# Performance work log

Measured on AMD Instinct MI355X. Metric: run time of the kernel, lower is better.

The kernel has to match this reference:

```python
import jax, jax.numpy as jnp
import numpy as np

# FPN level layout for a 1024x1024 input image
LEVEL_HW = [(128, 128), (64, 64), (32, 32), (16, 16), (8, 8)]
STRIDES = [8, 16, 32, 64, 128]
IMG = 1024.0
NUM_CLASSES = 80
SCORE_THRESH = 0.2
NMS_THRESH = 0.6
TOPK = 1000
DETS = 100
BATCH = 8
TOTAL = sum(h * w for h, w in LEVEL_HW)  # 21824


def _make_anchors():
    rows = []
    for (h, w), s in zip(LEVEL_HW, STRIDES):
        xs = (np.arange(w, dtype=np.float32) + 0.5) * s
        ys = (np.arange(h, dtype=np.float32) + 0.5) * s
        xx, yy = np.meshgrid(xs, ys, indexing='ij')  # x-major, matches transpose(2,3) flatten
        pts = np.stack([xx.ravel(), yy.ravel(), xx.ravel(), yy.ravel()], axis=1)
        rows.append(pts)
    return np.concatenate(rows, axis=0).astype(np.float32)


def setup_inputs() -> dict:
    key = jax.random.key(0)
    k1, k2, k3 = jax.random.split(key, 3)
    cls_logits = jax.random.normal(k1, (BATCH, TOTAL, NUM_CLASSES), dtype=jnp.float32)
    bbox_regression = jax.random.uniform(k2, (BATCH, TOTAL, 4), dtype=jnp.float32) * 64.0
    bbox_ctrness = jax.random.normal(k3, (BATCH, TOTAL, 1), dtype=jnp.float32)
    anchors = jnp.asarray(_make_anchors())
    return {"cls_logits": cls_logits, "bbox_regression": bbox_regression,
            "bbox_ctrness": bbox_ctrness, "anchors": anchors}


def _iou_matrix(b):
    # b: [N,4] -> [N,N] pairwise IoU
    area = jnp.clip(b[:, 2] - b[:, 0], 0) * jnp.clip(b[:, 3] - b[:, 1], 0)
    lt = jnp.maximum(b[:, None, :2], b[None, :, :2])
    rb = jnp.minimum(b[:, None, 2:], b[None, :, 2:])
    wh = jnp.clip(rb - lt, 0)
    inter = wh[..., 0] * wh[..., 1]
    union = area[:, None] + area[None, :] - inter
    return inter / jnp.maximum(union, 1e-9)


def _postprocess_one(logits, reg, ctr, anchors):
    boxes_l, scores_l, labels_l = [], [], []
    off = 0
    for (h, w) in LEVEL_HW:
        n = h * w
        lg = logits[off:off + n]          # [n, C]
        rg = reg[off:off + n]             # [n, 4]
        ct = ctr[off:off + n, 0]          # [n]
        an = anchors[off:off + n]         # [n, 4]
        vals = lg.max(axis=-1)
        cls = jnp.argmax(lg, axis=-1)
        sc = jnp.sqrt(jax.nn.sigmoid(vals) * jax.nn.sigmoid(ct))
        # masked threshold + top-k  ==  filter-then-topk of the original
        masked = jnp.where(sc > SCORE_THRESH, sc, -1.0)
        k = min(TOPK, n)
        tv, ti = jax.lax.top_k(masked, k)
        a = an[ti]
        r = rg[ti]
        cx = (a[:, 0] + a[:, 2]) * 0.5
        cy = (a[:, 1] + a[:, 3]) * 0.5
        bx = jnp.stack([cx - r[:, 0], cy - r[:, 1], cx + r[:, 2], cy + r[:, 3]], axis=-1)
        bx = jnp.clip(bx, 0.0, IMG)       # clip_boxes_to_image
        boxes_l.append(bx)
        scores_l.append(tv)
        labels_l.append(cls[ti])
        off += n
    boxes = jnp.concatenate(boxes_l, axis=0)    # [N,4], N=3320
    scores = jnp.concatenate(scores_l, axis=0)  # [N]
    labels = jnp.concatenate(labels_l, axis=0)  # [N]
    N = boxes.shape[0]
    valid = scores > SCORE_THRESH
    order = jnp.argsort(-scores)
    boxes = boxes[order]
    scores = scores[order]
    labels = labels[order]
    valid = valid[order]
    # batched_nms: offset boxes per class so cross-class IoU is 0
    boff = boxes + (labels.astype(boxes.dtype) * (IMG + 1.0))[:, None]
    iou = _iou_matrix(boff)
    idx = jnp.arange(N)
    def body(i, active):
        sup = (iou[i] > NMS_THRESH) & (idx > i) & active[i]
        return active & ~sup
    active = jax.lax.fori_loop(0, N, body, valid)
    fsc = jnp.where(active, scores, -jnp.inf)
    tv, ti = jax.lax.top_k(fsc, DETS)
    m = tv > SCORE_THRESH
    out_boxes = jnp.where(m[:, None], boxes[ti], 0.0)
    out_scores = jnp.where(m, tv, 0.0)
    out_labels = jnp.where(m, labels[ti], -1)
    return out_boxes, out_scores, out_labels


def reference(cls_logits, bbox_regression, bbox_ctrness, anchors):
    fn = lambda l, r, c: _postprocess_one(l, r, c, anchors)
    boxes, scores, labels = jax.vmap(fn)(cls_logits, bbox_regression, bbox_ctrness)
    return boxes, scores, labels
```

## Files before the change

kernel.cpp:

```cpp
#include <hip/hip_runtime.h>
#include <stdint.h>

typedef unsigned long long u64;
typedef unsigned int u32;

#define BATCH   8
#define TOTAL   21824
#define NCLS    80
#define NDET    100
#define IMGSZ   1024.0f
#define STHR    0.2f
#define NMST    0.6f
#define NBUCK   2048
#define BMAX    2015
#define KGLOB   1000
#define NLOC    22

__device__ __forceinline__ float sigm(float x) { return 1.0f / (1.0f + expf(-x)); }

__device__ __forceinline__ u32 mapKm(float s) {
    u32 u = __float_as_uint(s);
    u32 m = u ^ ((u & 0x80000000u) ? 0xFFFFFFFFu : 0x80000000u);
    return ~m;
}
__device__ __forceinline__ u64 makeKey(float s, u32 idx) {
    return (((u64)mapKm(s)) << 32) | (u64)idx;
}

__device__ __forceinline__ int bucketOfV(float s) {
    int b = (int)(__fmul_rn(__fsub_rn(1.0f, s), 2520.0f));
    return b > BMAX ? BMAX : b;
}

__device__ __forceinline__ bool suppress(float4 a, float4 c) {
    float aa = __fmul_rn(fmaxf(__fsub_rn(a.z, a.x), 0.f), fmaxf(__fsub_rn(a.w, a.y), 0.f));
    float ac = __fmul_rn(fmaxf(__fsub_rn(c.z, c.x), 0.f), fmaxf(__fsub_rn(c.w, c.y), 0.f));
    float ltx = fmaxf(a.x, c.x), lty = fmaxf(a.y, c.y);
    float rbx = fminf(a.z, c.z), rby = fminf(a.w, c.w);
    float iw = fmaxf(__fsub_rn(rbx, ltx), 0.f), ih = fmaxf(__fsub_rn(rby, lty), 0.f);
    float inter = __fmul_rn(iw, ih);
    float uni = __fsub_rn(__fadd_rn(aa, ac), inter);
    float iou = __fdiv_rn(inter, fmaxf(uni, 1e-9f));
    return iou > NMST;
}

__global__ __launch_bounds__(256) void zero_hist(u32* __restrict__ g) {
    ((uint4*)g)[blockIdx.x * 256 + threadIdx.x] = make_uint4(0u, 0u, 0u, 0u);
}

__global__ __launch_bounds__(256) void score_kernel(
        const float* __restrict__ logits, const float* __restrict__ ctr,
        float* __restrict__ mscore, int* __restrict__ mlabel,
        u32* __restrict__ ghist) {
    const int b = blockIdx.y;
    const int tid = threadIdx.x;
    const int wave = tid >> 6, lane = tid & 63;
    const int g = lane >> 2, j = lane & 3;
    const int rowBase = blockIdx.x * 256 + wave * 64;
#pragma unroll
    for (int t = 0; t < 4; t++) {
        int r = rowBase + 16 * t + g;
        bool valid = r < TOTAL;
        float best = -1e30f; int bi = 0;
        if (valid) {
            const float* rowp = logits + ((size_t)b * TOTAL + r) * NCLS + j * 4;
#pragma unroll
            for (int u = 0; u < 5; u++) {
                float4 v = *(const float4*)(rowp + u * 16);
                int c0 = u * 16 + j * 4;
                if (v.x > best) { best = v.x; bi = c0; }
                if (v.y > best) { best = v.y; bi = c0 + 1; }
                if (v.z > best) { best = v.z; bi = c0 + 2; }
                if (v.w > best) { best = v.w; bi = c0 + 3; }
            }
        }
#pragma unroll
        for (int off = 1; off <= 2; off <<= 1) {
            float ob = __shfl_xor(best, off);
            int obi = __shfl_xor(bi, off);
            if (ob > best || (ob == best && obi < bi)) { best = ob; bi = obi; }
        }
        if (valid && j == 0) {
            float c = ctr[(size_t)b * TOTAL + r];
            float sc = sqrtf(sigm(best) * sigm(c));
            bool pass = sc > STHR;
            mscore[(size_t)b * TOTAL + r] = pass ? sc : -1.0f;
            mlabel[(size_t)b * TOTAL + r] = bi;
            if (pass) atomicAdd(&ghist[(size_t)b * NBUCK + bucketOfV(sc)], 1u);
        }
    }
}

__global__ __launch_bounds__(1024) void nms_kernel(
        const float* __restrict__ mscore, const int* __restrict__ mlabel,
        const float* __restrict__ anchors, const float* __restrict__ reg,
        const u32* __restrict__ ghist, float* __restrict__ out) {
    __shared__ u32 cur[NBUCK];
    __shared__ u64 skey[2048];
    __shared__ u32 waveSum[16], waveOff[16];
    __shared__ u32 sh_B, sh_m;
    __shared__ int s_count;
    __shared__ int accI[NDET];
    __shared__ float4 accB[NDET];
    __shared__ float4 accR[NDET];
    __shared__ int wIdx[64];
    __shared__ float4 wb[64], wraw[64];
    __shared__ u64 wsup[64];
    __shared__ u32 s_rej32[2];

    const int b = blockIdx.x, tid = threadIdx.x;
    const int wave = tid >> 6, lane = tid & 63;
    const float* ms = mscore + (size_t)b * TOTAL;

    uint2 hv = ((const uint2*)(ghist + (size_t)b * NBUCK))[tid];

    float sv[NLOC];
#pragma unroll
    for (int k = 0; k < NLOC; k++) {
        int i = tid + (k << 10);
        sv[k] = (i < TOTAL) ? ms[i] : -1.0f;
    }

    u32 h0 = hv.x, h1 = hv.y;
    u32 s = h0 + h1;
    u32 incl = s;
    for (int o = 1; o < 64; o <<= 1) {
        u32 t2 = (u32)__shfl_up((int)incl, o);
        if (lane >= o) incl += t2;
    }
    if (lane == 63) waveSum[wave] = incl;
    __syncthreads();
    if (tid == 0) {
        u32 acc = 0;
#pragma unroll
        for (int w = 0; w < 16; w++) { waveOff[w] = acc; acc += waveSum[w]; }
        sh_m = acc;
        sh_B = (u32)BMAX;
        s_count = 0;
    }
    __syncthreads();
    const u32 E = waveOff[wave] + incl - s;
    if (E < KGLOB && KGLOB <= E + h0)            { sh_B = (u32)(2 * tid);     sh_m = E + h0; }
    else if (E + h0 < KGLOB && KGLOB <= E + h0 + h1) { sh_B = (u32)(2 * tid + 1); sh_m = E + h0 + h1; }
    cur[2 * tid] = E;
    cur[2 * tid + 1] = E + h0;
    __syncthreads();
    const int Bstar = (int)sh_B;

#pragma unroll
    for (int k = 0; k < NLOC; k++) {
        float s0 = sv[k];
        if (s0 > STHR) {
            int bk = bucketOfV(s0);
            if (bk <= Bstar) {
                int pos = (int)atomicAdd(&cur[bk], 1u);
                if (pos < 2048) skey[pos] = makeKey(s0, (u32)(tid + (k << 10)));
            }
        }
    }
    __syncthreads();

#pragma unroll
    for (int q = 0; q < 2; q++) {
        int bk = 2 * tid + q;
        u32 cnt = q ? h1 : h0;
        if (bk <= Bstar && cnt > 1) {
            int lo = (int)(q ? (E + h0) : E);
            int hi = lo + (int)cnt; if (hi > 2048) hi = 2048;
            for (int i2 = lo + 1; i2 < hi; i2++) {
                u64 key = skey[i2];
                int j2 = i2 - 1;
                while (j2 >= lo && skey[j2] > key) { skey[j2 + 1] = skey[j2]; j2--; }
                skey[j2 + 1] = key;
            }
        }
    }
    __syncthreads();
    int m = (int)sh_m; if (m > 2048) m = 2048;

    int count = 0, Ew = 0;
    while (true) {
        int take = m - Ew; if (take > 64) take = 64;
        if (take <= 0) break;

        if (tid < take) {
            int idx = (int)(skey[Ew + tid] & 0xFFFFFFFFu);
            float4 a = ((const float4*)anchors)[idx];
            float4 r = ((const float4*)reg)[(size_t)b * TOTAL + idx];
            float cx = (a.x + a.z) * 0.5f;
            float cy = (a.y + a.w) * 0.5f;
            float x1 = fminf(fmaxf(cx - r.x, 0.0f), IMGSZ);
            float y1 = fminf(fmaxf(cy - r.y, 0.0f), IMGSZ);
            float x2 = fminf(fmaxf(cx + r.z, 0.0f), IMGSZ);
            float y2 = fminf(fmaxf(cy + r.w, 0.0f), IMGSZ);
            float4 raw = make_float4(x1, y1, x2, y2);
            float off = (float)mlabel[(size_t)b * TOTAL + idx] * (IMGSZ + 1.0f);
            float4 ob = make_float4(__fadd_rn(x1, off), __fadd_rn(y1, off),
                                    __fadd_rn(x2, off), __fadd_rn(y2, off));
            wraw[tid] = raw; wb[tid] = ob; wIdx[tid] = idx;
        }
        if (tid < 2) s_rej32[tid] = 0;
        __syncthreads();

        {
            bool rej = false;
            if (lane < take) {
                for (int s2 = wave; s2 < count; s2 += 16) {
                    if (suppress(accB[s2], wb[lane])) { rej = true; break; }
                }
            }
            u64 mask = __ballot(rej);
            if (lane == 0 && mask) {
                u32 lo = (u32)mask, hi = (u32)(mask >> 32);
                if (lo) atomicOr(&s_rej32[0], lo);
                if (hi) atomicOr(&s_rej32[1], hi);
            }
        }
        for (int rr = wave; rr < take; rr += 16) {
            bool sp = false;
            if (lane < take && lane > rr) sp = suppress(wb[rr], wb[lane]);
            u64 mask = __ballot(sp);
            if (lane == 0) wsup[rr] = mask;
        }
        __syncthreads();

        if (wave == 0) {
            u64 supr = (lane < take) ? wsup[lane] : 0;
            u64 rejM = (u64)s_rej32[0] | ((u64)s_rej32[1] << 32);
            u64 aliveM = ((take >= 64) ? ~0ull : ((1ull << take) - 1ull)) & ~rejM;
            u64 accM = 0;
            for (int rr = 0; rr < take; rr++) {
                if ((aliveM >> rr) & 1) {
                    accM |= 1ull << rr;
                    u64 sr = __shfl(supr, rr);
                    aliveM &= ~sr;
                }
            }
            int na = __popcll(accM);
            int space = NDET - count;
            int takeA = na < space ? na : space;
            if (lane < take && ((accM >> lane) & 1)) {
                int pos = __popcll(accM & ((1ull << lane) - 1ull));
                if (pos < takeA) {
                    accI[count + pos] = wIdx[lane];
                    accB[count + pos] = wb[lane];
                    accR[count + pos] = wraw[lane];
                }
            }
            if (lane == 0) s_count = count + takeA;
        }
        __syncthreads();
        count = s_count;
        Ew += take;
        if (count >= NDET) break;
    }
    __syncthreads();

    for (int s2 = tid; s2 < NDET; s2 += 1024) {
        float4 bxv = make_float4(0.f, 0.f, 0.f, 0.f);
        float scv = 0.0f, lbv = -1.0f;
        if (s2 < count) {
            int idx = accI[s2];
            bxv = accR[s2];
            scv = ms[idx];
            lbv = (float)mlabel[(size_t)b * TOTAL + idx];
        }
        ((float4*)out)[b * NDET + s2] = bxv;
        out[BATCH * NDET * 4 + b * NDET + s2] = scv;
        out[BATCH * NDET * 4 + BATCH * NDET + b * NDET + s2] = lbv;
    }
}

extern "C" void kernel_launch(void* const* d_in, const int* in_sizes, int n_in,
                              void* d_out, int out_size, void* d_ws, size_t ws_size,
                              hipStream_t stream) {
    (void)in_sizes; (void)n_in; (void)out_size; (void)ws_size;
    const float* logits  = (const float*)d_in[0];
    const float* reg     = (const float*)d_in[1];
    const float* ctr     = (const float*)d_in[2];
    const float* anchors = (const float*)d_in[3];
    float* out = (float*)d_out;

    char* ws = (char*)d_ws;
    size_t off = 0;
    auto alloc = [&](size_t bytes) -> void* {
        off = (off + 255) & ~(size_t)255;
        void* p = ws + off;
        off += bytes;
        return p;
    };
    float* mscore = (float*)alloc((size_t)BATCH * TOTAL * 4);
    int*   mlabel = (int*)  alloc((size_t)BATCH * TOTAL * 4);
    u32*   ghist  = (u32*)  alloc((size_t)BATCH * NBUCK * 4);

    zero_hist<<<dim3((BATCH * NBUCK) / (256 * 4)), 256, 0, stream>>>(ghist);
    score_kernel<<<dim3((TOTAL + 255) / 256, BATCH), 256, 0, stream>>>(logits, ctr, mscore, mlabel, ghist);
    nms_kernel<<<BATCH, 1024, 0, stream>>>(mscore, mlabel, anchors, reg, ghist, out);
}
```

Baseline: 143.3 us.

## Prefetch top candidate boxes into LDS and fast-path greedy NMS acceptance

The candidate boxes for the first 1024 sorted candidates are decoded in parallel into shared memory up front, so the serial NMS loop no longer does a dependent global gather on every 64-wide chunk. The histogram is doubled to 4096 finer buckets, which shrinks the per-bucket insertion sort. Rejection masks are combined with per-wave stores plus a shuffle reduction instead of shared atomics. A fast path accepts a whole chunk when there is no suppression inside it. The cost is more LDS per block, about 36KB extra, and a larger histogram to zero and scan.

```diff
diff --git a/kernel.cpp b/kernel.cpp
--- a/kernel.cpp
+++ b/kernel.cpp
@@ -11,10 +11,11 @@
 #define IMGSZ   1024.0f
 #define STHR    0.2f
 #define NMST    0.6f
-#define NBUCK   2048
-#define BMAX    2015
+#define NBUCK   4096
+#define BMAX    4031
 #define KGLOB   1000
 #define NLOC    22
+#define PRE     1024
 
 __device__ __forceinline__ float sigm(float x) { return 1.0f / (1.0f + expf(-x)); }
 
@@ -23,12 +24,15 @@
     u32 m = u ^ ((u & 0x80000000u) ? 0xFFFFFFFFu : 0x80000000u);
     return ~m;
 }
+__device__ __forceinline__ float unmapKm(u32 km) {
+    return __uint_as_float((~km) ^ 0x80000000u);
+}
 __device__ __forceinline__ u64 makeKey(float s, u32 idx) {
     return (((u64)mapKm(s)) << 32) | (u64)idx;
 }
 
 __device__ __forceinline__ int bucketOfV(float s) {
-    int b = (int)(__fmul_rn(__fsub_rn(1.0f, s), 2520.0f));
+    int b = (int)(__fmul_rn(__fsub_rn(1.0f, s), 5040.0f));
     return b > BMAX ? BMAX : b;
 }
 
@@ -97,22 +101,29 @@
         const u32* __restrict__ ghist, float* __restrict__ out) {
     __shared__ u32 cur[NBUCK];
     __shared__ u64 skey[2048];
+    __shared__ float4 preB[PRE];
+    __shared__ float4 preR[PRE];
+    __shared__ int    preL[PRE];
     __shared__ u32 waveSum[16], waveOff[16];
     __shared__ u32 sh_B, sh_m;
     __shared__ int s_count;
-    __shared__ int accI[NDET];
     __shared__ float4 accB[NDET];
     __shared__ float4 accR[NDET];
-    __shared__ int wIdx[64];
+    __shared__ float  accS[NDET];
+    __shared__ int    accL[NDET];
     __shared__ float4 wb[64], wraw[64];
+    __shared__ int    wLab[64];
     __shared__ u64 wsup[64];
-    __shared__ u32 s_rej32[2];
+    __shared__ u64 sRej[16];
 
     const int b = blockIdx.x, tid = threadIdx.x;
     const int wave = tid >> 6, lane = tid & 63;
     const float* ms = mscore + (size_t)b * TOTAL;
-
-    uint2 hv = ((const uint2*)(ghist + (size_t)b * NBUCK))[tid];
+    const int* ml = mlabel + (size_t)b * TOTAL;
+    const float4* anch4 = (const float4*)anchors;
+    const float4* reg4 = ((const float4*)reg) + (size_t)b * TOTAL;
+
+    uint4 hv = ((const uint4*)(ghist + (size_t)b * NBUCK))[tid];
 
     float sv[NLOC];
 #pragma unroll
@@ -121,8 +132,8 @@
         sv[k] = (i < TOTAL) ? ms[i] : -1.0f;
     }
 
-    u32 h0 = hv.x, h1 = hv.y;
-    u32 s = h0 + h1;
+    u32 h0 = hv.x, h1 = hv.y, h2 = hv.z, h3 = hv.w;
+    u32 s = h0 + h1 + h2 + h3;
     u32 incl = s;
     for (int o = 1; o < 64; o <<= 1) {
         u32 t2 = (u32)__shfl_up((int)incl, o);
@@ -140,10 +151,15 @@
     }
     __syncthreads();
     const u32 E = waveOff[wave] + incl - s;
-    if (E < KGLOB && KGLOB <= E + h0)            { sh_B = (u32)(2 * tid);     sh_m = E + h0; }
-    else if (E + h0 < KGLOB && KGLOB <= E + h0 + h1) { sh_B = (u32)(2 * tid + 1); sh_m = E + h0 + h1; }
-    cur[2 * tid] = E;
-    cur[2 * tid + 1] = E + h0;
+    const u32 p1 = E + h0, p2 = p1 + h1, p3 = p2 + h2, p4 = p3 + h3;
+    if      (E  < KGLOB && KGLOB <= p1) { sh_B = (u32)(4 * tid);     sh_m = p1; }
+    else if (p1 < KGLOB && KGLOB <= p2) { sh_B = (u32)(4 * tid + 1); sh_m = p2; }
+    else if (p2 < KGLOB && KGLOB <= p3) { sh_B = (u32)(4 * tid + 2); sh_m = p3; }
+    else if (p3 < KGLOB && KGLOB <= p4) { sh_B = (u32)(4 * tid + 3); sh_m = p4; }
+    cur[4 * tid]     = E;
+    cur[4 * tid + 1] = p1;
+    cur[4 * tid + 2] = p2;
+    cur[4 * tid + 3] = p3;
     __syncthreads();
     const int Bstar = (int)sh_B;
 
@@ -161,11 +177,12 @@
     __syncthreads();
 
 #pragma unroll
-    for (int q = 0; q < 2; q++) {
-        int bk = 2 * tid + q;
-        u32 cnt = q ? h1 : h0;
+    for (int q = 0; q < 4; q++) {
+        int bk = 4 * tid + q;
+        u32 cnt = (q == 0) ? h0 : (q == 1) ? h1 : (q == 2) ? h2 : h3;
+        u32 lo0 = (q == 0) ? E  : (q == 1) ? p1 : (q == 2) ? p2 : p3;
         if (bk <= Bstar && cnt > 1) {
-            int lo = (int)(q ? (E + h0) : E);
+            int lo = (int)lo0;
             int hi = lo + (int)cnt; if (hi > 2048) hi = 2048;
             for (int i2 = lo + 1; i2 < hi; i2++) {
                 u64 key = skey[i2];
@@ -177,74 +194,111 @@
     }
     __syncthreads();
     int m = (int)sh_m; if (m > 2048) m = 2048;
+    const int Pm = m < PRE ? m : PRE;
+
+    for (int p = tid; p < Pm; p += 1024) {
+        u64 key = skey[p];
+        int idx = (int)(key & 0xFFFFFFFFu);
+        float4 a = anch4[idx];
+        float4 r = reg4[idx];
+        int lb = ml[idx];
+        float cx = (a.x + a.z) * 0.5f;
+        float cy = (a.y + a.w) * 0.5f;
+        float x1 = fminf(fmaxf(cx - r.x, 0.0f), IMGSZ);
+        float y1 = fminf(fmaxf(cy - r.y, 0.0f), IMGSZ);
+        float x2 = fminf(fmaxf(cx + r.z, 0.0f), IMGSZ);
+        float y2 = fminf(fmaxf(cy + r.w, 0.0f), IMGSZ);
+        float off = (float)lb * (IMGSZ + 1.0f);
+        preR[p] = make_float4(x1, y1, x2, y2);
+        preB[p] = make_float4(__fadd_rn(x1, off), __fadd_rn(y1, off),
+                              __fadd_rn(x2, off), __fadd_rn(y2, off));
+        preL[p] = lb;
+    }
+    __syncthreads();
 
     int count = 0, Ew = 0;
     while (true) {
         int take = m - Ew; if (take > 64) take = 64;
         if (take <= 0) break;
-
-        if (tid < take) {
-            int idx = (int)(skey[Ew + tid] & 0xFFFFFFFFu);
-            float4 a = ((const float4*)anchors)[idx];
-            float4 r = ((const float4*)reg)[(size_t)b * TOTAL + idx];
-            float cx = (a.x + a.z) * 0.5f;
-            float cy = (a.y + a.w) * 0.5f;
-            float x1 = fminf(fmaxf(cx - r.x, 0.0f), IMGSZ);
-            float y1 = fminf(fmaxf(cy - r.y, 0.0f), IMGSZ);
-            float x2 = fminf(fmaxf(cx + r.z, 0.0f), IMGSZ);
-            float y2 = fminf(fmaxf(cy + r.w, 0.0f), IMGSZ);
-            float4 raw = make_float4(x1, y1, x2, y2);
-            float off = (float)mlabel[(size_t)b * TOTAL + idx] * (IMGSZ + 1.0f);
-            float4 ob = make_float4(__fadd_rn(x1, off), __fadd_rn(y1, off),
-                                    __fadd_rn(x2, off), __fadd_rn(y2, off));
-            wraw[tid] = raw; wb[tid] = ob; wIdx[tid] = idx;
-        }
-        if (tid < 2) s_rej32[tid] = 0;
-        __syncthreads();
+        const bool ldsPath = (Ew + take <= Pm);
+
+        if (!ldsPath) {
+            if (tid < take) {
+                int idx = (int)(skey[Ew + tid] & 0xFFFFFFFFu);
+                float4 a = anch4[idx];
+                float4 r = reg4[idx];
+                int lb = ml[idx];
+                float cx = (a.x + a.z) * 0.5f;
+                float cy = (a.y + a.w) * 0.5f;
+                float x1 = fminf(fmaxf(cx - r.x, 0.0f), IMGSZ);
+                float y1 = fminf(fmaxf(cy - r.y, 0.0f), IMGSZ);
+                float x2 = fminf(fmaxf(cx + r.z, 0.0f), IMGSZ);
+                float y2 = fminf(fmaxf(cy + r.w, 0.0f), IMGSZ);
+                float off = (float)lb * (IMGSZ + 1.0f);
+                wraw[tid] = make_float4(x1, y1, x2, y2);
+                wb[tid] = make_float4(__fadd_rn(x1, off), __fadd_rn(y1, off),
+                                      __fadd_rn(x2, off), __fadd_rn(y2, off));
+                wLab[tid] = lb;
+            }
+            __syncthreads();
+        }
 
         {
+            float4 myB;
+            if (lane < take) myB = ldsPath ? preB[Ew + lane] : wb[lane];
             bool rej = false;
             if (lane < take) {
                 for (int s2 = wave; s2 < count; s2 += 16) {
-                    if (suppress(accB[s2], wb[lane])) { rej = true; break; }
+                    if (suppress(accB[s2], myB)) { rej = true; break; }
                 }
             }
             u64 mask = __ballot(rej);
-            if (lane == 0 && mask) {
-                u32 lo = (u32)mask, hi = (u32)(mask >> 32);
-                if (lo) atomicOr(&s_rej32[0], lo);
-                if (hi) atomicOr(&s_rej32[1], hi);
-            }
-        }
-        for (int rr = wave; rr < take; rr += 16) {
-            bool sp = false;
-            if (lane < take && lane > rr) sp = suppress(wb[rr], wb[lane]);
-            u64 mask = __ballot(sp);
-            if (lane == 0) wsup[rr] = mask;
+            if (lane == 0) sRej[wave] = mask;
+            for (int rr = wave; rr < take; rr += 16) {
+                float4 rB = ldsPath ? preB[Ew + rr] : wb[rr];
+                bool sp = (lane < take && lane > rr) ? suppress(rB, myB) : false;
+                u64 msk = __ballot(sp);
+                if (lane == 0) wsup[rr] = msk;
+            }
         }
         __syncthreads();
 
         if (wave == 0) {
-            u64 supr = (lane < take) ? wsup[lane] : 0;
-            u64 rejM = (u64)s_rej32[0] | ((u64)s_rej32[1] << 32);
-            u64 aliveM = ((take >= 64) ? ~0ull : ((1ull << take) - 1ull)) & ~rejM;
-            u64 accM = 0;
-            for (int rr = 0; rr < take; rr++) {
-                if ((aliveM >> rr) & 1) {
+            u64 rj = (lane < 16) ? sRej[lane] : 0ull;
+#pragma unroll
+            for (int o = 1; o < 64; o <<= 1) rj |= __shfl_xor(rj, o);
+            u64 supr = (lane < take) ? wsup[lane] : 0ull;
+            u64 validb = (take >= 64) ? ~0ull : ((1ull << take) - 1ull);
+            u64 aliveM = validb & ~rj;
+            u64 contrib = ((aliveM >> lane) & 1ull) ? supr : 0ull;
+            u64 U = contrib;
+#pragma unroll
+            for (int o = 1; o < 64; o <<= 1) U |= __shfl_xor(U, o);
+            int space = NDET - count;
+            u64 accM;
+            if ((U & aliveM) == 0ull) {
+                accM = aliveM;
+            } else {
+                u64 rem = aliveM; accM = 0ull;
+                while (rem) {
+                    int rr = __builtin_ctzll(rem);
                     accM |= 1ull << rr;
+                    if (__popcll(accM) >= space) break;
                     u64 sr = __shfl(supr, rr);
-                    aliveM &= ~sr;
+                    rem &= ~(1ull << rr);
+                    rem &= ~sr;
                 }
             }
             int na = __popcll(accM);
-            int space = NDET - count;
             int takeA = na < space ? na : space;
-            if (lane < take && ((accM >> lane) & 1)) {
+            if (lane < take && ((accM >> lane) & 1ull)) {
                 int pos = __popcll(accM & ((1ull << lane) - 1ull));
                 if (pos < takeA) {
-                    accI[count + pos] = wIdx[lane];
-                    accB[count + pos] = wb[lane];
-                    accR[count + pos] = wraw[lane];
+                    int o2 = count + pos;
+                    accB[o2] = ldsPath ? preB[Ew + lane] : wb[lane];
+                    accR[o2] = ldsPath ? preR[Ew + lane] : wraw[lane];
+                    accL[o2] = ldsPath ? preL[Ew + lane] : wLab[lane];
+                    accS[o2] = unmapKm((u32)(skey[Ew + lane] >> 32));
                 }
             }
             if (lane == 0) s_count = count + takeA;
@@ -260,10 +314,9 @@
         float4 bxv = make_float4(0.f, 0.f, 0.f, 0.f);
         float scv = 0.0f, lbv = -1.0f;
         if (s2 < count) {
-            int idx = accI[s2];
             bxv = accR[s2];
-            scv = ms[idx];
-            lbv = (float)mlabel[(size_t)b * TOTAL + idx];
+            scv = accS[s2];
+            lbv = (float)accL[s2];
         }
         ((float4*)out)[b * NDET + s2] = bxv;
         out[BATCH * NDET * 4 + b * NDET + s2] = scv;
```

New measurement: 133.0 us. 7.2% less time.
